# Kernel tuning notes

Measured on AMD Instinct MI355X. Metric: run time of the kernel, lower is better.

## Reference

```python
import jax, jax.numpy as jnp
import numpy as np
import math

B, S, D, H, WD = 8, 2048, 512, 8, 64
DK = D // H


def setup_inputs() -> dict:
    k = jax.random.key(0)
    ks = jax.random.split(k, 16)
    s = 0.02
    return {
        "query": jax.random.normal(ks[0], (B, S, D), jnp.float32),
        "key": jax.random.normal(ks[1], (B, S, D), jnp.float32),
        "value": jax.random.normal(ks[2], (B, S, D), jnp.float32),
        "mask": jax.random.randint(ks[3], (B, S), 0, 2, jnp.int32),
        "segment_weights": jax.random.uniform(ks[4], (B, S, S), jnp.float32),
        # torch Linear weights: [out_features, in_features]
        "Wq": jax.random.normal(ks[5], (D, D), jnp.float32) * s,
        "bq": jnp.zeros((D,), jnp.float32),
        "Wk": jax.random.normal(ks[6], (D, D), jnp.float32) * s,
        "bk": jnp.zeros((D,), jnp.float32),
        "Wv": jax.random.normal(ks[7], (D, D), jnp.float32) * s,
        "bv": jnp.zeros((D,), jnp.float32),
        "Wo": jax.random.normal(ks[8], (D, D), jnp.float32) * s,
        "bo": jnp.zeros((D,), jnp.float32),
        "Wl": jax.random.normal(ks[9], (WD, 1), jnp.float32) * 0.1,
        "bl": jnp.zeros((WD,), jnp.float32),
        "Wr": jax.random.normal(ks[10], (1, WD), jnp.float32) * 0.1,
        "br": jnp.zeros((1,), jnp.float32),
    }


def reference(query, key, value, mask, segment_weights,
              Wq, bq, Wk, bk, Wv, bv, Wo, bo, Wl, bl, Wr, br):
    nb = query.shape[0]
    # segment bias MLP: 1 -> WD -> 1 with leaky_relu(0.2)
    sw = 1.0 / jnp.log(jnp.float32(math.e) + segment_weights)  # [B,S,S]
    hmid = jax.nn.leaky_relu(sw[..., None] * Wl[:, 0] + bl, negative_slope=0.2)  # [B,S,S,WD]
    bias = (hmid @ Wr.T + br)[..., 0]  # [B,S,S]

    def proj(x, W, b):
        return (x @ W.T + b).reshape(nb, -1, H, DK).transpose(0, 2, 1, 3)  # [B,H,S,DK]

    q = proj(query, Wq, bq)
    k = proj(key, Wk, bk)
    v = proj(value, Wv, bv)

    scores = jnp.einsum("bhqd,bhkd->bhqk", q, k) / jnp.float32(math.sqrt(DK))
    scores = scores + bias[:, None]  # broadcast over heads
    # mask [B,S] -> [B,1,S,1]: masks query rows (as in original)
    scores = jnp.where(mask[:, None, :, None] == 0, jnp.float32(-1e9), scores)
    p = jax.nn.softmax(scores, axis=-1)
    x = jnp.einsum("bhqk,bhkd->bhqd", p, v)
    x = x.transpose(0, 2, 1, 3).reshape(nb, -1, H * DK)
    return x @ Wo.T + bo
```

## Files before the change

### kernel.cpp

```cpp
#include <hip/hip_runtime.h>
#include <stdint.h>

#define Bb 8
#define Ss 2048
#define Dd 512
#define Hh 8

typedef unsigned short u16;
typedef __attribute__((ext_vector_type(8))) short s16x8;
typedef __attribute__((ext_vector_type(4))) unsigned short u16x4;
typedef __attribute__((ext_vector_type(4))) float f32x4;

__device__ __forceinline__ u16 f2bf(float f){
  unsigned u = __float_as_uint(f);
  return (u16)((u + 0x7fffu + ((u>>16)&1u)) >> 16);
}

__device__ __forceinline__ void gl_lds16(const void* g, void* l){
  __builtin_amdgcn_global_load_lds((const __attribute__((address_space(1))) unsigned int*)g,
                                   (__attribute__((address_space(3))) unsigned int*)l, 16, 0, 0);
}

#define MFMA32(a,b,c) __builtin_amdgcn_mfma_f32_16x16x32_bf16(a,b,c,0,0,0)

__global__ __launch_bounds__(256) void castw(const float* __restrict__ a, const float* __restrict__ b,
                                             const float* __restrict__ c, const float* __restrict__ d,
                                             u16* __restrict__ o){
  int i = blockIdx.x*256 + threadIdx.x;
  const float* src = (i < 65536) ? a : (i < 131072) ? b : (i < 196608) ? c : d;
  int off = (i & 65535) << 2;
  f32x4 v = *(const f32x4*)(src + off);
  u16x4 r;
  #pragma unroll
  for(int j = 0; j < 4; j++) r[j] = f2bf(v[j]);
  *(u16x4*)(o + ((size_t)(i >> 16) << 18) + off) = r;
}

__global__ void prep(const float* __restrict__ Wl, const float* __restrict__ bl,
                     const float* __restrict__ Wr, const float* __restrict__ br,
                     float* __restrict__ consts){
  int w = threadIdx.x;
  float wl = Wl[w], blv = bl[w], wr = Wr[w];
  float h0 = 0.75f*wl + blv; h0 = h0 > 0.f ? h0 : 0.2f*h0;
  float h1 = 1.00f*wl + blv; h1 = h1 > 0.f ? h1 : 0.2f*h1;
  float f0 = wr*h0, f1 = wr*h1;
  #pragma unroll
  for(int off = 32; off > 0; off >>= 1){
    f0 += __shfl_down(f0, off);
    f1 += __shfl_down(f1, off);
  }
  if(w == 0){
    float brv = br[0];
    float F0 = f0 + brv, F1 = f1 + brv;
    float C1 = (F1 - F0) * 4.0f;
    float C0 = F0 - 0.75f*C1;
    consts[0] = C1 * 1.4426950408889634f;
    consts[1] = C0;
  }
}

template<int MODE>
__global__ __launch_bounds__(256) void gemm_t(const void* __restrict__ Ap, const u16* __restrict__ W,
                                              const float* __restrict__ bias, void* __restrict__ Cp){
  __shared__ __align__(16) u16 As[128*32];
  __shared__ __align__(16) u16 Bs[128*32];
  const int t = threadIdx.x;
  const int lane = t & 63, wv = t >> 6;
  const int quad = lane >> 4, l15 = lane & 15;
  const int m0 = blockIdx.x * 128, n0 = blockIdx.y * 128;
  const int R = (wv >> 1) * 64, Cc = (wv & 1) * 64;
  f32x4 acc[4][4] = {};
  for(int kb = 0; kb < 512; kb += 32){
    __syncthreads();
    #pragma unroll
    for(int i = 0; i < 2; i++){
      int u  = i*256 + t;
      int m  = u >> 2;
      int cc = (u & 3) ^ ((m >> 1) & 3);
      if (MODE == 2){
        gl_lds16((const u16*)Ap + (size_t)(m0 + m)*512 + kb + cc*8, As + (size_t)(i*256 + wv*64)*8);
      } else {
        const float* src = (const float*)Ap + (size_t)(m0 + m)*512 + kb + cc*8;
        f32x4 v0 = *(const f32x4*)src;
        f32x4 v1 = *(const f32x4*)(src + 4);
        s16x8 cv;
        #pragma unroll
        for(int r2 = 0; r2 < 4; r2++){ cv[r2] = (short)f2bf(v0[r2]); cv[4+r2] = (short)f2bf(v1[r2]); }
        *(s16x8*)(As + (size_t)u*8) = cv;
      }
      gl_lds16(W + (size_t)(n0 + m)*512 + kb + cc*8, Bs + (size_t)(i*256 + wv*64)*8);
    }
    __syncthreads();
    s16x8 af[4], bfr[4];
    #pragma unroll
    for(int mi = 0; mi < 4; mi++){
      int m = R + mi*16 + l15;
      int u = (m << 2) | (quad ^ ((m >> 1) & 3));
      af[mi] = *(const s16x8*)(As + (size_t)u*8);
    }
    #pragma unroll
    for(int ni = 0; ni < 4; ni++){
      int n = Cc + ni*16 + l15;
      int u = (n << 2) | (quad ^ ((n >> 1) & 3));
      bfr[ni] = *(const s16x8*)(Bs + (size_t)u*8);
    }
    #pragma unroll
    for(int mi = 0; mi < 4; mi++)
      #pragma unroll
      for(int ni = 0; ni < 4; ni++)
        acc[mi][ni] = MFMA32(af[mi], bfr[ni], acc[mi][ni]);
  }
  #pragma unroll
  for(int ni = 0; ni < 4; ni++){
    int col = n0 + Cc + ni*16 + l15;
    float bv = bias[col];
    #pragma unroll
    for(int mi = 0; mi < 4; mi++){
      int row0 = m0 + R + mi*16 + quad*4;
      #pragma unroll
      for(int r = 0; r < 4; r++){
        float v = acc[mi][ni][r] + bv;
        int row = row0 + r;
        if (MODE == 2)      ((float*)Cp)[(size_t)row*512 + col] = v;
        else if (MODE == 1) ((u16*)Cp)[(size_t)((row >> 11)*512 + col)*2048 + (size_t)(row & 2047)] = f2bf(v);
        else                ((u16*)Cp)[(size_t)row*512 + col] = f2bf(v);
      }
    }
  }
}

__global__ __launch_bounds__(512, 2) void attn(const u16* __restrict__ qp, const u16* __restrict__ kp,
                                               const u16* __restrict__ vt, const float* __restrict__ seg,
                                               const int* __restrict__ mask, const float* __restrict__ consts,
                                               u16* __restrict__ xo){
  __shared__ __align__(16) float bias_s[64*36];
  const int t = threadIdx.x;
  const int lane = t & 63, h = t >> 6;
  const int quad = lane >> 4, l15 = lane & 15;
  const int b = blockIdx.x >> 5, q0 = (blockIdx.x & 31) * 64;
  const float C1 = consts[0], C0 = consts[1];
  const int krA = 8*(l15 >> 2) + (l15 & 3);

  s16x8 qf[4][2];
  #pragma unroll
  for(int ni = 0; ni < 4; ni++){
    const u16* qrow = qp + (size_t)(b*Ss + q0 + ni*16 + l15)*Dd + h*64;
    qf[ni][0] = *(const s16x8*)(qrow + quad*8);
    qf[ni][1] = *(const s16x8*)(qrow + 32 + quad*8);
  }
  float mk[4];
  #pragma unroll
  for(int ni = 0; ni < 4; ni++)
    mk[ni] = (mask[b*Ss + q0 + ni*16 + l15] == 0) ? 0.0f : 1.0f;

  f32x4 ot[4][4] = {};
  float lsum[4] = {0.f, 0.f, 0.f, 0.f};

  const int sq = t >> 3, sk = (t & 7) * 4;
  const float* segrow = seg + ((size_t)b*Ss + (size_t)(q0 + sq))*Ss + sk;

  for(int k0 = 0; k0 < Ss; k0 += 32){
    __syncthreads();
    {
      f32x4 raw = *(const f32x4*)(segrow + k0);
      f32x4 bv;
      #pragma unroll
      for(int j = 0; j < 4; j++){
        float x = 2.718281828459045f + raw[j];
        bv[j] = C1 * __builtin_amdgcn_rcpf(__log2f(x)) + C0;
      }
      *(f32x4*)(bias_s + sq*36 + sk) = bv;
    }
    __syncthreads();

    f32x4 st[2][4] = {};
    #pragma unroll
    for(int ks = 0; ks < 2; ks++){
      s16x8 kf[2];
      #pragma unroll
      for(int mi = 0; mi < 2; mi++)
        kf[mi] = *(const s16x8*)(kp + (size_t)(b*Ss + k0 + krA + mi*4)*Dd + h*64 + ks*32 + quad*8);
      #pragma unroll
      for(int mi = 0; mi < 2; mi++)
        #pragma unroll
        for(int ni = 0; ni < 4; ni++)
          st[mi][ni] = MFMA32(kf[mi], qf[ni][ks], st[mi][ni]);
    }

    s16x8 pf8[4];
    #pragma unroll
    for(int mi = 0; mi < 2; mi++)
      #pragma unroll
      for(int ni = 0; ni < 4; ni++){
        f32x4 bb = *(const f32x4*)(bias_s + (ni*16 + l15)*36 + quad*8 + mi*4);
        f32x4 s = st[mi][ni] * 0.125f + bb;
        s *= mk[ni];
        #pragma unroll
        for(int r = 0; r < 4; r++){
          float sv = fminf(fmaxf(s[r], -30.f), 30.f);
          float p = __expf(sv);
          lsum[ni] += p;
          pf8[ni][mi*4 + r] = (short)f2bf(p);
        }
      }

    #pragma unroll
    for(int mi2 = 0; mi2 < 4; mi2++){
      s16x8 vf = *(const s16x8*)(vt + (size_t)(b*Dd + h*64 + mi2*16 + l15)*Ss + k0 + quad*8);
      #pragma unroll
      for(int ni = 0; ni < 4; ni++)
        ot[mi2][ni] = MFMA32(vf, pf8[ni], ot[mi2][ni]);
    }
  }

  float rl[4];
  #pragma unroll
  for(int ni = 0; ni < 4; ni++){
    float l = lsum[ni];
    l += __shfl_xor(l, 16);
    l += __shfl_xor(l, 32);
    rl[ni] = 1.0f / l;
  }

  #pragma unroll
  for(int ni = 0; ni < 4; ni++)
    #pragma unroll
    for(int mi2 = 0; mi2 < 4; mi2++){
      u16x4 o;
      #pragma unroll
      for(int r = 0; r < 4; r++) o[r] = f2bf(ot[mi2][ni][r] * rl[ni]);
      *(u16x4*)(xo + (size_t)(b*Ss + q0 + ni*16 + l15)*Dd + h*64 + mi2*16 + quad*4) = o;
    }
}

extern "C" void kernel_launch(void* const* d_in, const int* in_sizes, int n_in,
                              void* d_out, int out_size, void* d_ws, size_t ws_size,
                              hipStream_t stream){
  const float* query = (const float*)d_in[0];
  const float* key   = (const float*)d_in[1];
  const float* value = (const float*)d_in[2];
  const int*   mask  = (const int*)d_in[3];
  const float* seg   = (const float*)d_in[4];
  const float* Wq = (const float*)d_in[5];  const float* bq = (const float*)d_in[6];
  const float* Wk = (const float*)d_in[7];  const float* bk = (const float*)d_in[8];
  const float* Wv = (const float*)d_in[9];  const float* bv = (const float*)d_in[10];
  const float* Wo = (const float*)d_in[11]; const float* bo = (const float*)d_in[12];
  const float* Wl = (const float*)d_in[13]; const float* bl = (const float*)d_in[14];
  const float* Wr = (const float*)d_in[15]; const float* br = (const float*)d_in[16];

  char* ws = (char*)d_ws;
  float* consts = (float*)ws;
  u16* Wc  = (u16*)(ws + 4096);
  u16* qp  = (u16*)(ws + ((size_t)4  << 20));
  u16* kp  = (u16*)(ws + ((size_t)20 << 20));
  u16* vt  = (u16*)(ws + ((size_t)36 << 20));
  u16* xo  = qp;
  const size_t WN = (size_t)512*512;

  castw<<<1024, 256, 0, stream>>>(Wq, Wk, Wv, Wo, Wc);
  prep<<<1, 64, 0, stream>>>(Wl, bl, Wr, br, consts);
  gemm_t<0><<<dim3(128,4), 256, 0, stream>>>(query, Wc + 0*WN, bq, qp);
  gemm_t<0><<<dim3(128,4), 256, 0, stream>>>(key,   Wc + 1*WN, bk, kp);
  gemm_t<1><<<dim3(128,4), 256, 0, stream>>>(value, Wc + 2*WN, bv, vt);
  attn<<<256, 512, 0, stream>>>(qp, kp, vt, seg, mask, consts, xo);
  gemm_t<2><<<dim3(128,4), 256, 0, stream>>>(xo, Wc + 3*WN, bo, d_out);
}
```

Baseline: 553.7 us.

## Halve attention query tile, double-buffer segment bias, and pack bf16 conversions

The attention kernel now handles 32 query rows per block instead of 64, launches 512 blocks with a 4-blocks-per-CU occupancy hint, and remaps block IDs so neighbouring blocks cover different batches. The segment-weight bias is double-buffered in LDS and the next tile is prefetched into registers, which drops one barrier per iteration and hides the global-load latency. The scalar bf16 rounding is replaced with the packed v_cvt_pk_bf16_f32 instruction. The aim is more parallelism and less stall on the 128MB segment-weight stream. The cost is that each key/value tile is now loaded by twice as many blocks.

New measurement: 599.2 us. 1.08x slower.

```diff
diff --git a/kernel.cpp b/kernel.cpp
--- a/kernel.cpp
+++ b/kernel.cpp
@@ -10,10 +10,17 @@
 typedef __attribute__((ext_vector_type(8))) short s16x8;
 typedef __attribute__((ext_vector_type(4))) unsigned short u16x4;
 typedef __attribute__((ext_vector_type(4))) float f32x4;
+typedef __attribute__((ext_vector_type(2))) float f32x2;
 
 __device__ __forceinline__ u16 f2bf(float f){
   unsigned u = __float_as_uint(f);
   return (u16)((u + 0x7fffu + ((u>>16)&1u)) >> 16);
+}
+
+__device__ __forceinline__ unsigned cvtpk_bf16(float lo, float hi){
+  unsigned r;
+  asm("v_cvt_pk_bf16_f32 %0, %1, %2" : "=v"(r) : "v"(lo), "v"(hi));
+  return r;
 }
 
 __device__ __forceinline__ void gl_lds16(const void* g, void* l){
@@ -129,51 +136,52 @@
   }
 }
 
-__global__ __launch_bounds__(512, 2) void attn(const u16* __restrict__ qp, const u16* __restrict__ kp,
+__global__ __launch_bounds__(512, 4) void attn(const u16* __restrict__ qp, const u16* __restrict__ kp,
                                                const u16* __restrict__ vt, const float* __restrict__ seg,
                                                const int* __restrict__ mask, const float* __restrict__ consts,
                                                u16* __restrict__ xo){
-  __shared__ __align__(16) float bias_s[64*36];
+  __shared__ __align__(16) float bias_s[2][32*36];
   const int t = threadIdx.x;
   const int lane = t & 63, h = t >> 6;
   const int quad = lane >> 4, l15 = lane & 15;
-  const int b = blockIdx.x >> 5, q0 = (blockIdx.x & 31) * 64;
+  const int id = (blockIdx.x & 7) * 64 + (blockIdx.x >> 3);
+  const int b = id >> 6, q0 = (id & 63) * 32;
   const float C1 = consts[0], C0 = consts[1];
   const int krA = 8*(l15 >> 2) + (l15 & 3);
 
-  s16x8 qf[4][2];
-  #pragma unroll
-  for(int ni = 0; ni < 4; ni++){
+  s16x8 qf[2][2];
+  #pragma unroll
+  for(int ni = 0; ni < 2; ni++){
     const u16* qrow = qp + (size_t)(b*Ss + q0 + ni*16 + l15)*Dd + h*64;
     qf[ni][0] = *(const s16x8*)(qrow + quad*8);
     qf[ni][1] = *(const s16x8*)(qrow + 32 + quad*8);
   }
-  float mk[4];
-  #pragma unroll
-  for(int ni = 0; ni < 4; ni++)
+  float mk[2];
+  #pragma unroll
+  for(int ni = 0; ni < 2; ni++)
     mk[ni] = (mask[b*Ss + q0 + ni*16 + l15] == 0) ? 0.0f : 1.0f;
 
-  f32x4 ot[4][4] = {};
-  float lsum[4] = {0.f, 0.f, 0.f, 0.f};
-
-  const int sq = t >> 3, sk = (t & 7) * 4;
+  f32x4 ot[4][2] = {};
+  float lsum[2] = {0.f, 0.f};
+
+  const int sq = t >> 4, sk = (t & 15) * 2;
   const float* segrow = seg + ((size_t)b*Ss + (size_t)(q0 + sq))*Ss + sk;
 
+  f32x2 raw = *(const f32x2*)(segrow);
+  f32x2 bvreg;
+  #pragma unroll
+  for(int j = 0; j < 2; j++){
+    float x = 2.718281828459045f + raw[j];
+    bvreg[j] = C1 * __builtin_amdgcn_rcpf(__log2f(x)) + C0;
+  }
+
   for(int k0 = 0; k0 < Ss; k0 += 32){
+    float* bs = bias_s[(k0 >> 5) & 1];
+    *(f32x2*)(bs + sq*36 + sk) = bvreg;
+    if (k0 + 32 < Ss) raw = *(const f32x2*)(segrow + k0 + 32);
     __syncthreads();
-    {
-      f32x4 raw = *(const f32x4*)(segrow + k0);
-      f32x4 bv;
-      #pragma unroll
-      for(int j = 0; j < 4; j++){
-        float x = 2.718281828459045f + raw[j];
-        bv[j] = C1 * __builtin_amdgcn_rcpf(__log2f(x)) + C0;
-      }
-      *(f32x4*)(bias_s + sq*36 + sk) = bv;
-    }
-    __syncthreads();
-
-    f32x4 st[2][4] = {};
+
+    f32x4 st[2][2] = {};
     #pragma unroll
     for(int ks = 0; ks < 2; ks++){
       s16x8 kf[2];
@@ -183,39 +191,49 @@
       #pragma unroll
       for(int mi = 0; mi < 2; mi++)
         #pragma unroll
-        for(int ni = 0; ni < 4; ni++)
+        for(int ni = 0; ni < 2; ni++)
           st[mi][ni] = MFMA32(kf[mi], qf[ni][ks], st[mi][ni]);
     }
 
-    s16x8 pf8[4];
+    union { unsigned u[4]; s16x8 v; } P[2];
     #pragma unroll
     for(int mi = 0; mi < 2; mi++)
       #pragma unroll
-      for(int ni = 0; ni < 4; ni++){
-        f32x4 bb = *(const f32x4*)(bias_s + (ni*16 + l15)*36 + quad*8 + mi*4);
+      for(int ni = 0; ni < 2; ni++){
+        f32x4 bb = *(const f32x4*)(bs + (ni*16 + l15)*36 + quad*8 + mi*4);
         f32x4 s = st[mi][ni] * 0.125f + bb;
         s *= mk[ni];
+        float p[4];
         #pragma unroll
         for(int r = 0; r < 4; r++){
           float sv = fminf(fmaxf(s[r], -30.f), 30.f);
-          float p = __expf(sv);
-          lsum[ni] += p;
-          pf8[ni][mi*4 + r] = (short)f2bf(p);
+          p[r] = __expf(sv);
+          lsum[ni] += p[r];
         }
+        P[ni].u[mi*2 + 0] = cvtpk_bf16(p[0], p[1]);
+        P[ni].u[mi*2 + 1] = cvtpk_bf16(p[2], p[3]);
       }
 
     #pragma unroll
     for(int mi2 = 0; mi2 < 4; mi2++){
       s16x8 vf = *(const s16x8*)(vt + (size_t)(b*Dd + h*64 + mi2*16 + l15)*Ss + k0 + quad*8);
       #pragma unroll
-      for(int ni = 0; ni < 4; ni++)
-        ot[mi2][ni] = MFMA32(vf, pf8[ni], ot[mi2][ni]);
-    }
-  }
-
-  float rl[4];
-  #pragma unroll
-  for(int ni = 0; ni < 4; ni++){
+      for(int ni = 0; ni < 2; ni++)
+        ot[mi2][ni] = MFMA32(vf, P[ni].v, ot[mi2][ni]);
+    }
+
+    if (k0 + 32 < Ss){
+      #pragma unroll
+      for(int j = 0; j < 2; j++){
+        float x = 2.718281828459045f + raw[j];
+        bvreg[j] = C1 * __builtin_amdgcn_rcpf(__log2f(x)) + C0;
+      }
+    }
+  }
+
+  float rl[2];
+  #pragma unroll
+  for(int ni = 0; ni < 2; ni++){
     float l = lsum[ni];
     l += __shfl_xor(l, 16);
     l += __shfl_xor(l, 32);
@@ -223,7 +241,7 @@
   }
 
   #pragma unroll
-  for(int ni = 0; ni < 4; ni++)
+  for(int ni = 0; ni < 2; ni++)
     #pragma unroll
     for(int mi2 = 0; mi2 < 4; mi2++){
       u16x4 o;
@@ -262,6 +280,6 @@
   gemm_t<0><<<dim3(128,4), 256, 0, stream>>>(query, Wc + 0*WN, bq, qp);
   gemm_t<0><<<dim3(128,4), 256, 0, stream>>>(key,   Wc + 1*WN, bk, kp);
   gemm_t<1><<<dim3(128,4), 256, 0, stream>>>(value, Wc + 2*WN, bv, vt);
-  attn<<<256, 512, 0, stream>>>(qp, kp, vt, seg, mask, consts, xo);
+  attn<<<512, 512, 0, stream>>>(qp, kp, vt, seg, mask, consts, xo);
   gemm_t<2><<<dim3(128,4), 256, 0, stream>>>(xo, Wc + 3*WN, bo, d_out);
 }
```
